# Performance work log

Measured on AMD Instinct MI355X. Metric: run time of the kernel, lower is better.

The kernel has to match this reference:

```python
import jax, jax.numpy as jnp
import numpy as np

TOP_K = 6          # num_experts_per_tok
N_GROUP = 8        # n_group
TOPK_GROUP = 3     # topk_group
ROUTED_SCALING = 1.0  # routed_scaling_factor


def setup_inputs() -> dict:
    key = jax.random.key(0)
    ks = jax.random.split(key, 6)
    M, H, N, E = 1024, 1024, 1024, 16   # tokens, hidden, moe_intermediate, n_routed_experts
    I_SH = 2 * N                        # n_shared_experts * moe_intermediate_size
    s = lambda k, shape, sc: jax.random.normal(k, shape, dtype=jnp.float32) * sc
    return {
        'hidden_states': s(ks[0], (M, H), 1.0),
        'gate_w': s(ks[1], (E, H), 0.02),            # router gate weight
        'w1': s(ks[2], (E, 2 * N, H), 0.02),         # per-expert fused gate+up proj
        'w2': s(ks[3], (E, H, N), 0.02),             # per-expert down proj
        'shared_gate_up': s(ks[4], (2 * I_SH, H), 0.02),  # shared experts gate+up (stacked dim 0)
        'shared_down': s(ks[5], (H, I_SH), 0.02),
    }


def _grouped_topk(logits, topk, n_group, topk_group):
    # Faithful to grouped_topk(): softmax -> per-group max -> top groups -> masked top-k experts.
    M, E = logits.shape
    scores = jax.nn.softmax(logits, axis=-1)                      # [M, E]
    group_scores = scores.reshape(M, n_group, E // n_group).max(-1)  # [M, G]
    _, gidx = jax.lax.top_k(group_scores, topk_group)             # [M, topk_group]
    gmask = jnp.sum(jax.nn.one_hot(gidx, n_group, dtype=scores.dtype), axis=1)  # [M, G]
    smask = jnp.repeat(gmask, E // n_group, axis=1)               # [M, E]
    tmp = jnp.where(smask > 0, scores, 0.0)
    topk_w, topk_ids = jax.lax.top_k(tmp, topk)                   # [M, topk]
    # norm_topk_prob = False -> no renormalization
    return topk_w, topk_ids


def reference(hidden_states, gate_w, w1, w2, shared_gate_up, shared_down):
    M, H = hidden_states.shape
    E = w1.shape[0]
    N = w2.shape[2]
    # --- routing ---
    logits = hidden_states @ gate_w.T                             # [M, E]
    topk_w, topk_ids = _grouped_topk(logits, TOP_K, N_GROUP, TOPK_GROUP)
    # scatter top-k weights into a dense [M, E] combine matrix (top_k ids are distinct)
    comb = jnp.zeros((M, E), hidden_states.dtype).at[
        jnp.arange(M)[:, None], topk_ids].add(topk_w)
    # --- fused_experts math (dense-over-experts emulation of the grouped GEMM) ---
    h = jnp.einsum('mh,efh->emf', hidden_states, w1)              # [E, M, 2N]
    g = jax.nn.silu(h[..., :N]) * h[..., N:]                      # silu_and_mul -> [E, M, N]
    out_e = jnp.einsum('emn,ehn->emh', g, w2)                     # [E, M, H]
    routed = jnp.einsum('emh,me->mh', out_e, comb) * ROUTED_SCALING
    # --- shared experts (DeepseekV2MLP, silu) ---
    gu = hidden_states @ shared_gate_up.T                         # [M, 2*I_SH]
    I = shared_down.shape[1]
    shared = (jax.nn.silu(gu[:, :I]) * gu[:, I:]) @ shared_down.T # [M, H]
    return routed + shared
```

## Files before the change

kernel.cpp:

```cpp
#include <hip/hip_runtime.h>
#include <hip/hip_bf16.h>


#define M_TOK 1024
#define HDIM  1024
#define NEXP  16
#define NMOE  1024
#define NSH   2048

using bf16x8 = __attribute__((ext_vector_type(8))) short;
using f32x4  = __attribute__((ext_vector_type(4))) float;

static __device__ __forceinline__ short f2b(float x) {
  __hip_bfloat16 b = __float2bfloat16(x);
  return __builtin_bit_cast(short, b);
}
static __device__ __forceinline__ float b2f(short s) {
  return __bfloat162float(__builtin_bit_cast(__hip_bfloat16, s));
}

static __device__ __forceinline__ uint4 pack8(float4 a, float4 b) {
  union { short s[8]; uint4 u; } r;
  r.s[0] = f2b(a.x); r.s[1] = f2b(a.y); r.s[2] = f2b(a.z); r.s[3] = f2b(a.w);
  r.s[4] = f2b(b.x); r.s[5] = f2b(b.y); r.s[6] = f2b(b.z); r.s[7] = f2b(b.w);
  return r.u;
}

static __device__ __forceinline__ int swz(int row, int chunk) {
  return (row << 7) + (((chunk ^ row) & 7) << 4);
}

__global__ __launch_bounds__(256)
void k_router(const float* __restrict__ hs, const float* __restrict__ gw,
              float* __restrict__ comb, unsigned* __restrict__ maskbuf) {
  int wave = threadIdx.x >> 6, lane = threadIdx.x & 63;
  int tok = blockIdx.x * 4 + wave;
  const float* hrow = hs + (size_t)tok * HDIM;
  float acc[16];
#pragma unroll
  for (int e = 0; e < 16; e++) acc[e] = 0.f;
  for (int h0 = 0; h0 < HDIM; h0 += 64) {
    float x = hrow[h0 + lane];
#pragma unroll
    for (int e = 0; e < 16; e++) acc[e] = fmaf(x, gw[e * HDIM + h0 + lane], acc[e]);
  }
#pragma unroll
  for (int e = 0; e < 16; e++) {
    float v = acc[e];
#pragma unroll
    for (int off = 32; off; off >>= 1) v += __shfl_xor(v, off);
    acc[e] = v;
  }
  float mx = acc[0];
#pragma unroll
  for (int e = 1; e < 16; e++) mx = fmaxf(mx, acc[e]);
  float sum = 0.f;
#pragma unroll
  for (int e = 0; e < 16; e++) { acc[e] = __expf(acc[e] - mx); sum += acc[e]; }
  float inv = 1.f / sum;
#pragma unroll
  for (int e = 0; e < 16; e++) acc[e] *= inv;
  float gs[8];
#pragma unroll
  for (int g = 0; g < 8; g++) gs[g] = fmaxf(acc[2 * g], acc[2 * g + 1]);
  unsigned gmask = 0;
  for (int t = 0; t < 3; t++) {
    int best = 0; float bv = -1.f;
#pragma unroll
    for (int g = 0; g < 8; g++) {
      bool take = (((gmask >> g) & 1u) == 0u) && (gs[g] > bv);
      bv = take ? gs[g] : bv;
      best = take ? g : best;
    }
    gmask |= 1u << best;
  }
  unsigned emask = 0;
#pragma unroll
  for (int g = 0; g < 8; g++) if ((gmask >> g) & 1u) emask |= 3u << (2 * g);
  if (lane < 16) comb[tok * 16 + lane] = ((emask >> lane) & 1u) ? acc[lane] : 0.f;
  if (lane == 0) maskbuf[tok] = emask;
}

__global__ __launch_bounds__(1024)
void k_build_lists(const unsigned* __restrict__ maskbuf, const float* __restrict__ comb,
                   int* __restrict__ lists, int* __restrict__ counts,
                   int* __restrict__ offsets, int* __restrict__ tok2row,
                   float* __restrict__ tokw) {
  int e = threadIdx.x >> 6, lane = threadIdx.x & 63;
  int cnt = 0;
  for (int c = 0; c < 16; c++) {
    int tok = c * 64 + lane;
    bool sel = (maskbuf[tok] >> e) & 1u;
    unsigned long long b = __ballot(sel);
    if (sel) {
      int pos = cnt + __popcll(b & ((1ull << lane) - 1ull));
      lists[e * 1024 + pos] = tok;
    }
    cnt += __popcll(b);
  }
  for (int i = cnt + lane; i < 1024; i += 64) lists[e * 1024 + i] = 0;
  if (lane == 0) counts[e] = cnt;
  __syncthreads();
  if (threadIdx.x == 0) {
    int run = 0;
    for (int ee = 0; ee < 16; ee++) { offsets[ee] = run; run += counts[ee]; }
  }
  __syncthreads();
  int base = offsets[e], n = counts[e];
  for (int i = lane; i < n; i += 64) {
    int tok = lists[e * 1024 + i];
    unsigned em = maskbuf[tok];
    int slot = __popc(em & ((1u << e) - 1u));
    tok2row[tok * 6 + slot] = base + i;
    tokw[tok * 6 + slot] = comb[tok * 16 + e];
  }
}

__global__ __launch_bounds__(256)
void k_mlp1(const float* __restrict__ A, const float* __restrict__ Wr,
            const float* __restrict__ Ws, __hip_bfloat16* __restrict__ Gr,
            __hip_bfloat16* __restrict__ Gs,
            const int* __restrict__ lists, const int* __restrict__ counts,
            const int* __restrict__ offsets) {
  int z = blockIdx.z;
  bool sh = (z >= NEXP);
  int e = sh ? 0 : z;
  int N = sh ? NSH : NMOE;
  int n0 = blockIdx.x * 64 + (sh ? (z - NEXP) * 1024 : 0);
  int m0 = blockIdx.y * 128;
  int count = sh ? M_TOK : counts[e];
  if (m0 >= count) return;
  int gbase = (sh ? 0 : offsets[e]) + m0;
  const float* We = sh ? Ws : (Wr + (size_t)e * (2 * (size_t)NMOE) * HDIM);
  __hip_bfloat16* G = sh ? Gs : Gr;

  __shared__ short sA[128 * 64];
  __shared__ short sB[128 * 64];
  __shared__ int sTok[128];
  char* cA = (char*)sA; char* cB = (char*)sB;

  int tid = threadIdx.x;
  if (tid < 128) sTok[tid] = sh ? (m0 + tid) : lists[e * 1024 + m0 + tid];
  __syncthreads();

  int rg = tid >> 3, ca = tid & 7;
  const float* pA[4]; const float* pB[4];
#pragma unroll
  for (int p = 0; p < 4; p++) {
    int row = p * 32 + rg;
    pA[p] = A + (size_t)sTok[row] * HDIM + ca * 8;
    int brow = (row < 64) ? (n0 + row) : (N + n0 + row - 64);
    pB[p] = We + (size_t)brow * HDIM + ca * 8;
  }

  int lane = tid & 63, wave = tid >> 6;
  int wm = wave >> 1, wn = wave & 1;
  int lrow = lane & 15, lquad = lane >> 4;

  f32x4 acc1[4][2] = {};
  f32x4 acc2[4][2] = {};

  for (int k0 = 0; k0 < HDIM; k0 += 64) {
    float4 a0[4], a1[4], b0[4], b1[4];
#pragma unroll
    for (int p = 0; p < 4; p++) {
      a0[p] = *reinterpret_cast<const float4*>(pA[p] + k0);
      a1[p] = *reinterpret_cast<const float4*>(pA[p] + k0 + 4);
      b0[p] = *reinterpret_cast<const float4*>(pB[p] + k0);
      b1[p] = *reinterpret_cast<const float4*>(pB[p] + k0 + 4);
    }
    __syncthreads();
#pragma unroll
    for (int p = 0; p < 4; p++) {
      int row = p * 32 + rg;
      *reinterpret_cast<uint4*>(cA + swz(row, ca)) = pack8(a0[p], a1[p]);
      *reinterpret_cast<uint4*>(cB + swz(row, ca)) = pack8(b0[p], b1[p]);
    }
    __syncthreads();
#pragma unroll
    for (int ks = 0; ks < 2; ks++) {
      bf16x8 af[4], bg[2], bu[2];
#pragma unroll
      for (int mi = 0; mi < 4; mi++)
        af[mi] = *reinterpret_cast<const bf16x8*>(cA + swz(wm * 64 + mi * 16 + lrow, ks * 4 + lquad));
#pragma unroll
      for (int ni = 0; ni < 2; ni++) {
        bg[ni] = *reinterpret_cast<const bf16x8*>(cB + swz(wn * 32 + ni * 16 + lrow, ks * 4 + lquad));
        bu[ni] = *reinterpret_cast<const bf16x8*>(cB + swz(64 + wn * 32 + ni * 16 + lrow, ks * 4 + lquad));
      }
#pragma unroll
      for (int mi = 0; mi < 4; mi++)
#pragma unroll
        for (int ni = 0; ni < 2; ni++) {
          acc1[mi][ni] = __builtin_amdgcn_mfma_f32_16x16x32_bf16(af[mi], bg[ni], acc1[mi][ni], 0, 0, 0);
          acc2[mi][ni] = __builtin_amdgcn_mfma_f32_16x16x32_bf16(af[mi], bu[ni], acc2[mi][ni], 0, 0, 0);
        }
    }
  }
#pragma unroll
  for (int mi = 0; mi < 4; mi++)
#pragma unroll
    for (int r = 0; r < 4; r++) {
      int li = wm * 64 + mi * 16 + lquad * 4 + r;
      if (m0 + li < count) {
#pragma unroll
        for (int ni = 0; ni < 2; ni++) {
          float x = acc1[mi][ni][r], y = acc2[mi][ni][r];
          float gv = (x / (1.f + __expf(-x))) * y;
          G[(size_t)(gbase + li) * N + (n0 + wn * 32 + ni * 16 + lrow)] = __float2bfloat16(gv);
        }
      }
    }
}

#define EPS 136
__global__ __launch_bounds__(256)
void k_mlp2(const __hip_bfloat16* __restrict__ Gr, const __hip_bfloat16* __restrict__ Gs,
            const float* __restrict__ Wr, const float* __restrict__ Ws,
            __hip_bfloat16* __restrict__ Or, float* __restrict__ out,
            const int* __restrict__ counts, const int* __restrict__ offsets) {
  int z = blockIdx.z;
  bool sh = (z >= NEXP);
  int e = sh ? 0 : z;
  int K = sh ? NSH : NMOE;
  int h0 = blockIdx.x * 128;
  int m0 = blockIdx.y * 64;
  int count = sh ? M_TOK : counts[e];
  if (m0 >= count) return;
  int abase = (sh ? 0 : offsets[e]) + m0;
  const __hip_bfloat16* Gm = sh ? Gs : Gr;
  const float* We = sh ? Ws : (Wr + (size_t)e * (size_t)HDIM * NMOE);

  __shared__ short smem[12288];
  char* cA = (char*)smem;
  char* cB = (char*)(smem + 4096);

  int tid = threadIdx.x;
  int rA = tid >> 2, ca2 = tid & 3;
  const __hip_bfloat16* pA = Gm + (size_t)(abase + rA) * K + ca2 * 8;
  int rgB = tid >> 3, cb = tid & 7;
  const float* pB[4];
#pragma unroll
  for (int p = 0; p < 4; p++)
    pB[p] = We + (size_t)(h0 + p * 32 + rgB) * K + cb * 8;

  int lane = tid & 63, wave = tid >> 6;
  int wm = wave >> 1, wn = wave & 1;
  int lrow = lane & 15, lquad = lane >> 4;

  f32x4 acc[2][4] = {};

  for (int k0 = 0; k0 < K; k0 += 64) {
    uint4 ua0 = *reinterpret_cast<const uint4*>(pA + k0);
    uint4 ua1 = *reinterpret_cast<const uint4*>(pA + k0 + 32);
    float4 b0[4], b1[4];
#pragma unroll
    for (int p = 0; p < 4; p++) {
      b0[p] = *reinterpret_cast<const float4*>(pB[p] + k0);
      b1[p] = *reinterpret_cast<const float4*>(pB[p] + k0 + 4);
    }
    __syncthreads();
    *reinterpret_cast<uint4*>(cA + swz(rA, ca2)) = ua0;
    *reinterpret_cast<uint4*>(cA + swz(rA, ca2 + 4)) = ua1;
#pragma unroll
    for (int p = 0; p < 4; p++)
      *reinterpret_cast<uint4*>(cB + swz(p * 32 + rgB, cb)) = pack8(b0[p], b1[p]);
    __syncthreads();
#pragma unroll
    for (int ks = 0; ks < 2; ks++) {
      bf16x8 af[2], bfr[4];
#pragma unroll
      for (int i = 0; i < 2; i++)
        af[i] = *reinterpret_cast<const bf16x8*>(cA + swz(wm * 32 + i * 16 + lrow, ks * 4 + lquad));
#pragma unroll
      for (int i = 0; i < 4; i++)
        bfr[i] = *reinterpret_cast<const bf16x8*>(cB + swz(wn * 64 + i * 16 + lrow, ks * 4 + lquad));
#pragma unroll
      for (int mi = 0; mi < 2; mi++)
#pragma unroll
        for (int ni = 0; ni < 4; ni++)
          acc[mi][ni] = __builtin_amdgcn_mfma_f32_16x16x32_bf16(af[mi], bfr[ni], acc[mi][ni], 0, 0, 0);
    }
  }
  __syncthreads();

  if (!sh) {
    short* epi = smem;
#pragma unroll
    for (int mi = 0; mi < 2; mi++)
#pragma unroll
      for (int ni = 0; ni < 4; ni++)
#pragma unroll
        for (int r = 0; r < 4; r++) {
          int row = wm * 32 + mi * 16 + lquad * 4 + r;
          int col = wn * 64 + ni * 16 + lrow;
          epi[row * EPS + col] = f2b(acc[mi][ni][r]);
        }
    __syncthreads();
    int row = tid >> 2, c16 = tid & 3;
    bool ok = (m0 + row) < count;
    size_t obase = (size_t)(abase + row) * HDIM + h0;
    if (ok) {
#pragma unroll
      for (int j = 0; j < 4; j++) {
        int chunk = c16 + 4 * j;
        *reinterpret_cast<uint4*>(Or + obase + chunk * 8) =
            *reinterpret_cast<const uint4*>(epi + row * EPS + chunk * 8);
      }
    }
  } else {
    float* epi32 = reinterpret_cast<float*>(smem);
#pragma unroll
    for (int p = 0; p < 2; p++) {
      if (wm == p) {
#pragma unroll
        for (int mi = 0; mi < 2; mi++)
#pragma unroll
          for (int ni = 0; ni < 4; ni++)
#pragma unroll
            for (int r = 0; r < 4; r++) {
              int row = mi * 16 + lquad * 4 + r;
              int col = wn * 64 + ni * 16 + lrow;
              epi32[row * EPS + col] = acc[mi][ni][r];
            }
      }
      __syncthreads();
      int row = tid >> 3, c = tid & 7;
      size_t obase = (size_t)(m0 + p * 32 + row) * HDIM + h0;
#pragma unroll
      for (int j = 0; j < 4; j++) {
        int chunk = c + 8 * j;
        *reinterpret_cast<float4*>(out + obase + chunk * 4) =
            *reinterpret_cast<const float4*>(epi32 + row * EPS + chunk * 4);
      }
      __syncthreads();
    }
  }
}

__global__ __launch_bounds__(256)
void k_combine(const __hip_bfloat16* __restrict__ Or, const int* __restrict__ tok2row,
               const float* __restrict__ tokw, float* __restrict__ out) {
  int tok = blockIdx.x;
  int c4 = threadIdx.x * 4;
  int rows[6]; float w[6];
#pragma unroll
  for (int k = 0; k < 6; k++) {
    rows[k] = tok2row[tok * 6 + k];
    w[k] = tokw[tok * 6 + k];
  }
  float* op = out + (size_t)tok * HDIM + c4;
  float4 o = *reinterpret_cast<float4*>(op);
#pragma unroll
  for (int k = 0; k < 6; k++) {
    short4 v = *reinterpret_cast<const short4*>(Or + (size_t)rows[k] * HDIM + c4);
    o.x = fmaf(w[k], b2f(v.x), o.x);
    o.y = fmaf(w[k], b2f(v.y), o.y);
    o.z = fmaf(w[k], b2f(v.z), o.z);
    o.w = fmaf(w[k], b2f(v.w), o.w);
  }
  *reinterpret_cast<float4*>(op) = o;
}

extern "C" void kernel_launch(void* const* d_in, const int* in_sizes, int n_in,
                              void* d_out, int out_size, void* d_ws, size_t ws_size,
                              hipStream_t stream) {
  const float* hs  = (const float*)d_in[0];
  const float* gw  = (const float*)d_in[1];
  const float* w1  = (const float*)d_in[2];
  const float* w2  = (const float*)d_in[3];
  const float* sgu = (const float*)d_in[4];
  const float* sd  = (const float*)d_in[5];
  float* out = (float*)d_out;
  char* ws = (char*)d_ws;

  float*    comb    = (float*)(ws + 0);
  unsigned* maskbuf = (unsigned*)(ws + 65536);
  int*      lists   = (int*)(ws + 69632);
  int*      counts  = (int*)(ws + 135168);
  int*      offsets = (int*)(ws + 135232);
  int*      tok2row = (int*)(ws + 139264);
  float*    tokw    = (float*)(ws + 163840);
  __hip_bfloat16* Gr = (__hip_bfloat16*)(ws + 262144);
  __hip_bfloat16* Gs = (__hip_bfloat16*)(ws + 13107200);
  __hip_bfloat16* Or = (__hip_bfloat16*)(ws + 17301504);
  if (ws_size < (size_t)(17301504 + 12845056)) return;

  k_router<<<dim3(256), dim3(256), 0, stream>>>(hs, gw, comb, maskbuf);
  k_build_lists<<<dim3(1), dim3(1024), 0, stream>>>(maskbuf, comb, lists, counts,
                                                    offsets, tok2row, tokw);
  k_mlp1<<<dim3(16, 8, 18), dim3(256), 0, stream>>>(hs, w1, sgu, Gr, Gs,
                                                    lists, counts, offsets);
  k_mlp2<<<dim3(8, 16, 17), dim3(256), 0, stream>>>(Gr, Gs, w2, sd, Or, out,
                                                    counts, offsets);
  k_combine<<<dim3(1024), dim3(256), 0, stream>>>(Or, tok2row, tokw, out);
}
```

Baseline: 180.2 us.

## Pre-gather bf16 activations and register-prefetch next K tile in MLP GEMMs

Adds a prep kernel that converts hidden states to bf16 and writes a gathered, expert-sorted bf16 copy using a new row-to-token map. The first MLP kernel then reads contiguous bf16 rows instead of gathering and converting fp32 tokens in every tile. Both MLP GEMMs now load the next K tile's global data into registers while the current tile's MFMAs run. The cost is an extra launch plus extra global reads and writes for the gathered copy, and higher register pressure from the prefetch buffers.

```diff
diff --git a/kernel.cpp b/kernel.cpp
--- a/kernel.cpp
+++ b/kernel.cpp
@@ -85,7 +85,7 @@
 void k_build_lists(const unsigned* __restrict__ maskbuf, const float* __restrict__ comb,
                    int* __restrict__ lists, int* __restrict__ counts,
                    int* __restrict__ offsets, int* __restrict__ tok2row,
-                   float* __restrict__ tokw) {
+                   float* __restrict__ tokw, int* __restrict__ row2tok) {
   int e = threadIdx.x >> 6, lane = threadIdx.x & 63;
   int cnt = 0;
   for (int c = 0; c < 16; c++) {
@@ -113,15 +113,32 @@
     int slot = __popc(em & ((1u << e) - 1u));
     tok2row[tok * 6 + slot] = base + i;
     tokw[tok * 6 + slot] = comb[tok * 16 + e];
+    row2tok[base + i] = tok;
   }
 }
 
 __global__ __launch_bounds__(256)
-void k_mlp1(const float* __restrict__ A, const float* __restrict__ Wr,
-            const float* __restrict__ Ws, __hip_bfloat16* __restrict__ Gr,
-            __hip_bfloat16* __restrict__ Gs,
-            const int* __restrict__ lists, const int* __restrict__ counts,
-            const int* __restrict__ offsets) {
+void k_prep(const float* __restrict__ hs, const int* __restrict__ row2tok,
+            __hip_bfloat16* __restrict__ hb, __hip_bfloat16* __restrict__ Ab) {
+  int r = blockIdx.x, t = threadIdx.x;
+  if (r < M_TOK) {
+    float4 v = *reinterpret_cast<const float4*>(hs + (size_t)r * HDIM + t * 4);
+    short4 s; s.x = f2b(v.x); s.y = f2b(v.y); s.z = f2b(v.z); s.w = f2b(v.w);
+    *reinterpret_cast<short4*>(hb + (size_t)r * HDIM + t * 4) = s;
+  } else {
+    int row = r - M_TOK;
+    int tok = row2tok[row];
+    float4 v = *reinterpret_cast<const float4*>(hs + (size_t)tok * HDIM + t * 4);
+    short4 s; s.x = f2b(v.x); s.y = f2b(v.y); s.z = f2b(v.z); s.w = f2b(v.w);
+    *reinterpret_cast<short4*>(Ab + (size_t)row * HDIM + t * 4) = s;
+  }
+}
+
+__global__ __launch_bounds__(256)
+void k_mlp1(const __hip_bfloat16* __restrict__ Ab, const __hip_bfloat16* __restrict__ hb,
+            const float* __restrict__ Wr, const float* __restrict__ Ws,
+            __hip_bfloat16* __restrict__ Gr, __hip_bfloat16* __restrict__ Gs,
+            const int* __restrict__ counts, const int* __restrict__ offsets) {
   int z = blockIdx.z;
   bool sh = (z >= NEXP);
   int e = sh ? 0 : z;
@@ -132,23 +149,21 @@
   if (m0 >= count) return;
   int gbase = (sh ? 0 : offsets[e]) + m0;
   const float* We = sh ? Ws : (Wr + (size_t)e * (2 * (size_t)NMOE) * HDIM);
+  const __hip_bfloat16* Abase = sh ? (hb + (size_t)m0 * HDIM)
+                                   : (Ab + (size_t)gbase * HDIM);
   __hip_bfloat16* G = sh ? Gs : Gr;
 
   __shared__ short sA[128 * 64];
   __shared__ short sB[128 * 64];
-  __shared__ int sTok[128];
   char* cA = (char*)sA; char* cB = (char*)sB;
 
   int tid = threadIdx.x;
-  if (tid < 128) sTok[tid] = sh ? (m0 + tid) : lists[e * 1024 + m0 + tid];
-  __syncthreads();
-
   int rg = tid >> 3, ca = tid & 7;
-  const float* pA[4]; const float* pB[4];
+  const __hip_bfloat16* pA[4]; const float* pB[4];
 #pragma unroll
   for (int p = 0; p < 4; p++) {
     int row = p * 32 + rg;
-    pA[p] = A + (size_t)sTok[row] * HDIM + ca * 8;
+    pA[p] = Abase + (size_t)row * HDIM + ca * 8;
     int brow = (row < 64) ? (n0 + row) : (N + n0 + row - 64);
     pB[p] = We + (size_t)brow * HDIM + ca * 8;
   }
@@ -160,23 +175,28 @@
   f32x4 acc1[4][2] = {};
   f32x4 acc2[4][2] = {};
 
+  uint4 ra[4]; float4 rb0[4], rb1[4];
+#define LOAD_AB1(kk)                                                      \
+  {                                                                       \
+    _Pragma("unroll") for (int p = 0; p < 4; p++) {                       \
+      ra[p]  = *reinterpret_cast<const uint4*>(pA[p] + (kk));             \
+      rb0[p] = *reinterpret_cast<const float4*>(pB[p] + (kk));            \
+      rb1[p] = *reinterpret_cast<const float4*>(pB[p] + (kk) + 4);        \
+    }                                                                     \
+  }
+  LOAD_AB1(0);
+
   for (int k0 = 0; k0 < HDIM; k0 += 64) {
-    float4 a0[4], a1[4], b0[4], b1[4];
-#pragma unroll
-    for (int p = 0; p < 4; p++) {
-      a0[p] = *reinterpret_cast<const float4*>(pA[p] + k0);
-      a1[p] = *reinterpret_cast<const float4*>(pA[p] + k0 + 4);
-      b0[p] = *reinterpret_cast<const float4*>(pB[p] + k0);
-      b1[p] = *reinterpret_cast<const float4*>(pB[p] + k0 + 4);
-    }
     __syncthreads();
 #pragma unroll
     for (int p = 0; p < 4; p++) {
       int row = p * 32 + rg;
-      *reinterpret_cast<uint4*>(cA + swz(row, ca)) = pack8(a0[p], a1[p]);
-      *reinterpret_cast<uint4*>(cB + swz(row, ca)) = pack8(b0[p], b1[p]);
+      *reinterpret_cast<uint4*>(cA + swz(row, ca)) = ra[p];
+      *reinterpret_cast<uint4*>(cB + swz(row, ca)) = pack8(rb0[p], rb1[p]);
     }
     __syncthreads();
+    int kn = (k0 + 64 < HDIM) ? (k0 + 64) : k0;
+    LOAD_AB1(kn);
 #pragma unroll
     for (int ks = 0; ks < 2; ks++) {
       bf16x8 af[4], bg[2], bu[2];
@@ -250,15 +270,19 @@
 
   f32x4 acc[2][4] = {};
 
+  uint4 ua0, ua1; float4 b0[4], b1[4];
+#define LOAD_AB2(kk)                                                      \
+  {                                                                       \
+    ua0 = *reinterpret_cast<const uint4*>(pA + (kk));                     \
+    ua1 = *reinterpret_cast<const uint4*>(pA + (kk) + 32);                \
+    _Pragma("unroll") for (int p = 0; p < 4; p++) {                       \
+      b0[p] = *reinterpret_cast<const float4*>(pB[p] + (kk));             \
+      b1[p] = *reinterpret_cast<const float4*>(pB[p] + (kk) + 4);         \
+    }                                                                     \
+  }
+  LOAD_AB2(0);
+
   for (int k0 = 0; k0 < K; k0 += 64) {
-    uint4 ua0 = *reinterpret_cast<const uint4*>(pA + k0);
-    uint4 ua1 = *reinterpret_cast<const uint4*>(pA + k0 + 32);
-    float4 b0[4], b1[4];
-#pragma unroll
-    for (int p = 0; p < 4; p++) {
-      b0[p] = *reinterpret_cast<const float4*>(pB[p] + k0);
-      b1[p] = *reinterpret_cast<const float4*>(pB[p] + k0 + 4);
-    }
     __syncthreads();
     *reinterpret_cast<uint4*>(cA + swz(rA, ca2)) = ua0;
     *reinterpret_cast<uint4*>(cA + swz(rA, ca2 + 4)) = ua1;
@@ -266,6 +290,8 @@
     for (int p = 0; p < 4; p++)
       *reinterpret_cast<uint4*>(cB + swz(p * 32 + rgB, cb)) = pack8(b0[p], b1[p]);
     __syncthreads();
+    int kn = (k0 + 64 < K) ? (k0 + 64) : k0;
+    LOAD_AB2(kn);
 #pragma unroll
     for (int ks = 0; ks < 2; ks++) {
       bf16x8 af[2], bfr[4];
@@ -381,16 +407,20 @@
   int*      offsets = (int*)(ws + 135232);
   int*      tok2row = (int*)(ws + 139264);
   float*    tokw    = (float*)(ws + 163840);
+  int*      row2tok = (int*)(ws + 188416);
   __hip_bfloat16* Gr = (__hip_bfloat16*)(ws + 262144);
   __hip_bfloat16* Gs = (__hip_bfloat16*)(ws + 13107200);
+  __hip_bfloat16* hb = (__hip_bfloat16*)(ws + 17301504);
+  __hip_bfloat16* Ab = (__hip_bfloat16*)(ws + 19398656);
   __hip_bfloat16* Or = (__hip_bfloat16*)(ws + 17301504);
-  if (ws_size < (size_t)(17301504 + 12845056)) return;
+  if (ws_size < (size_t)(19398656 + 12845056)) return;
 
   k_router<<<dim3(256), dim3(256), 0, stream>>>(hs, gw, comb, maskbuf);
   k_build_lists<<<dim3(1), dim3(1024), 0, stream>>>(maskbuf, comb, lists, counts,
-                                                    offsets, tok2row, tokw);
-  k_mlp1<<<dim3(16, 8, 18), dim3(256), 0, stream>>>(hs, w1, sgu, Gr, Gs,
-                                                    lists, counts, offsets);
+                                                    offsets, tok2row, tokw, row2tok);
+  k_prep<<<dim3(M_TOK + 6144), dim3(256), 0, stream>>>(hs, row2tok, hb, Ab);
+  k_mlp1<<<dim3(16, 8, 18), dim3(256), 0, stream>>>(Ab, hb, w1, sgu, Gr, Gs,
+                                                    counts, offsets);
   k_mlp2<<<dim3(8, 16, 17), dim3(256), 0, stream>>>(Gr, Gs, w2, sd, Or, out,
                                                     counts, offsets);
   k_combine<<<dim3(1024), dim3(256), 0, stream>>>(Or, tok2row, tokw, out);
```

New measurement: 268.9 us. 49.2% more time.
